# Kernel tuning notes

Hardware: AMD Instinct MI355X
Metric: run time of the kernel (lower is better)

Reference implementation:

```python
import jax, jax.numpy as jnp
import numpy as np

N_NODES = 50000
N_EDGES = 800000
N_FEAT = 256
HIDDEN = 128
N_CLASSES = 40


def gcn_conv(x, src, dst, W, b, n_nodes):
    """PyG GCNConv: add self-loops, symmetric normalization, x@W then scatter-add."""
    h = x @ W  # [N, out]
    loop = jnp.arange(n_nodes, dtype=src.dtype)
    s = jnp.concatenate([src, loop])  # [E+N]
    d = jnp.concatenate([dst, loop])
    deg = jax.ops.segment_sum(jnp.ones_like(d, dtype=h.dtype), d, num_segments=n_nodes)
    dinv = jnp.where(deg > 0, jax.lax.rsqrt(deg), 0.0)
    norm = dinv[s] * dinv[d]  # [E+N]
    msg = h[s] * norm[:, None]  # gather + scale
    out = jax.ops.segment_sum(msg, d, num_segments=n_nodes)  # scatter-add to targets
    return out + b


def setup_inputs() -> dict:
    key = jax.random.key(0)
    k1, k2, k3, k4 = jax.random.split(key, 4)
    x = jax.random.normal(k1, (N_NODES, N_FEAT), dtype=jnp.float32)
    edge_index = jax.random.randint(k2, (2, N_EDGES), 0, N_NODES, dtype=jnp.int32)
    # Glorot-style init for conv weights, zero bias (PyG default)
    W1 = jax.random.normal(k3, (N_FEAT, HIDDEN), dtype=jnp.float32) * (1.0 / np.sqrt(N_FEAT))
    b1 = jnp.zeros((HIDDEN,), dtype=jnp.float32)
    W2 = jax.random.normal(k4, (HIDDEN, N_CLASSES), dtype=jnp.float32) * (1.0 / np.sqrt(HIDDEN))
    b2 = jnp.zeros((N_CLASSES,), dtype=jnp.float32)
    return {"x": x, "edge_index": edge_index, "W1": W1, "b1": b1, "W2": W2, "b2": b2}


def reference(x, edge_index, W1, b1, W2, b2):
    # eval mode: dropout is identity
    src, dst = edge_index[0], edge_index[1]
    h = gcn_conv(x, src, dst, W1, b1, N_NODES)
    h = jax.nn.relu(h)
    h = gcn_conv(h, src, dst, W2, b2, N_NODES)
    return jax.nn.log_softmax(h, axis=1)
```

## Files before the change

kernel.cpp:

```cpp
#include <hip/hip_runtime.h>
#include <cstdint>

#define N_NODES 50000
#define N_EDGES 800000
#define N_FEAT 256
#define HIDDEN 128
#define N_CLASSES 40
#define NBUCKET 196
#define EPB 3125
#define ROWS_PAD 50048
#define H2S 64

typedef __attribute__((ext_vector_type(8))) short bf16x8;
typedef __attribute__((ext_vector_type(4))) float f32x4;

__device__ inline ushort f2bf(float f) {
    union { float f; uint u; } v; v.f = f;
    uint u = v.u;
    u += 0x7fff + ((u >> 16) & 1);
    return (ushort)(u >> 16);
}
__device__ inline float bflo(uint u) {
    union { uint u; float f; } v; v.u = u << 16; return v.f;
}
__device__ inline float bfhi(uint u) {
    union { uint u; float f; } v; v.u = u & 0xffff0000u; return v.f;
}


__global__ void hist_repack(const int* __restrict__ dst, int* __restrict__ histT,
                            const float* __restrict__ W1, const float* __restrict__ W2,
                            ushort* __restrict__ Bp1, ushort* __restrict__ Bp2) {
    __shared__ int h[NBUCKET];
    int blk = blockIdx.x, t = threadIdx.x;
    int gid = blk * 256 + t;
    if (gid < 32768) {
        int j = gid & 7, lane = (gid >> 3) & 63, kt = (gid >> 9) & 7, nt = gid >> 12;
        int k = kt * 32 + (lane >> 4) * 8 + j;
        int n = nt * 16 + (lane & 15);
        Bp1[gid] = f2bf(W1[k * HIDDEN + n]);
    } else if (gid < 32768 + 6144) {
        int i2 = gid - 32768;
        int j = i2 & 7, lane = (i2 >> 3) & 63, kt = (i2 >> 9) & 3, nt = i2 >> 11;
        int k = kt * 32 + (lane >> 4) * 8 + j;
        int n = nt * 16 + (lane & 15);
        Bp2[i2] = (n < N_CLASSES) ? f2bf(W2[k * N_CLASSES + n]) : (ushort)0;
    }
    if (t < NBUCKET) h[t] = 0;
    __syncthreads();
    int base = blk * EPB;
    for (int i = t; i < EPB; i += 256)
        atomicAdd(&h[dst[base + i] >> 8], 1);
    __syncthreads();
    if (t < NBUCKET) histT[t * 256 + blk] = h[t];
}


__global__ void scan_a(const int* __restrict__ in, int* __restrict__ incl,
                       int* __restrict__ bsum) {
    __shared__ int s[256];
    int blk = blockIdx.x, t = threadIdx.x;
    int i = blk * 256 + t;
    s[t] = in[i];
    __syncthreads();
    for (int off = 1; off < 256; off <<= 1) {
        int t2 = 0;
        if (t >= off) t2 = s[t - off];
        __syncthreads();
        s[t] += t2;
        __syncthreads();
    }
    incl[i] = s[t];
    if (t == 255) bsum[blk] = s[255];
}

__global__ void scan_c(int* __restrict__ incl, const int* __restrict__ in,
                       const int* __restrict__ bsum) {
    __shared__ int s[256];
    int blk = blockIdx.x, t = threadIdx.x;
    s[t] = (t < NBUCKET) ? bsum[t] : 0;
    __syncthreads();
    for (int off = 1; off < 256; off <<= 1) {
        int t2 = 0;
        if (t >= off) t2 = s[t - off];
        __syncthreads();
        s[t] += t2;
        __syncthreads();
    }
    int base = (blk > 0) ? s[blk - 1] : 0;
    int i = blk * 256 + t;
    incl[i] = incl[i] - in[i] + base;
}


__global__ void partition_k(const int* __restrict__ src, const int* __restrict__ dst,
                            const int* __restrict__ poff, uint* __restrict__ ebuf) {
    __shared__ int base[NBUCKET];
    __shared__ int cur[NBUCKET];
    int blk = blockIdx.x, t = threadIdx.x;
    if (t < NBUCKET) { base[t] = poff[t * 256 + blk]; cur[t] = 0; }
    __syncthreads();
    int eb = blk * EPB;
    for (int i = t; i < EPB; i += 256) {
        int d = dst[eb + i], s = src[eb + i];
        int bk = d >> 8;
        int p = base[bk] + atomicAdd(&cur[bk], 1);
        ebuf[p] = ((uint)d << 16) | (uint)s;
    }
}


__global__ void bucket_csr(const uint* __restrict__ ebuf, const int* __restrict__ poff,
                           int* __restrict__ deg, float* __restrict__ dinv,
                           int* __restrict__ rowptr, int* __restrict__ esrc) {
    __shared__ int cnt[256];
    __shared__ int s[256];
    __shared__ int exc[256];
    __shared__ int cur[256];
    int b = blockIdx.x, t = threadIdx.x;
    cnt[t] = 0;
    cur[t] = 0;
    __syncthreads();
    int beg = poff[b * 256];
    int end = (b < NBUCKET - 1) ? poff[(b + 1) * 256] : N_EDGES;
    for (int i = beg + t; i < end; i += 256)
        atomicAdd(&cnt[(ebuf[i] >> 16) & 255], 1);
    __syncthreads();
    int d = cnt[t];
    s[t] = d;
    __syncthreads();
    for (int off = 1; off < 256; off <<= 1) {
        int t2 = 0;
        if (t >= off) t2 = s[t - off];
        __syncthreads();
        s[t] += t2;
        __syncthreads();
    }
    exc[t] = s[t] - d;
    int node = b * 256 + t;
    if (node < N_NODES) {
        deg[node] = d;
        dinv[node] = rsqrtf((float)(d + 1));
        rowptr[node] = beg + exc[t];
    }
    __syncthreads();
    for (int i = beg + t; i < end; i += 256) {
        uint u = ebuf[i];
        int dl = (int)(u >> 16) & 255;
        int pos = beg + exc[dl] + atomicAdd(&cur[dl], 1);
        esrc[pos] = (int)(u & 0xffffu);
    }
}


#define XS_STRIDE 264

__global__ __launch_bounds__(256) void gemm1_mfma(const float* __restrict__ x,
                                                  const ushort* __restrict__ Bp,
                                                  ushort* __restrict__ h1b) {
    __shared__ ushort xs[64 * XS_STRIDE];
    int t = threadIdx.x;
    int row0 = blockIdx.x * 64;
#pragma unroll
    for (int i = 0; i < 16; ++i) {
        int idx = t + i * 256;
        int r = idx >> 6, kg = idx & 63;
        int row = row0 + r;
        float4 v = make_float4(0.f, 0.f, 0.f, 0.f);
        if (row < N_NODES) v = *(const float4*)(x + (size_t)row * N_FEAT + kg * 4);
        ushort4 u;
        u.x = f2bf(v.x); u.y = f2bf(v.y); u.z = f2bf(v.z); u.w = f2bf(v.w);
        *(ushort4*)(&xs[r * XS_STRIDE + kg * 4]) = u;
    }
    __syncthreads();
    int lane = t & 63, w = t >> 6;
    int r = lane & 15, q = lane >> 4;
    f32x4 acc[8] = {};
    for (int kt = 0; kt < 8; ++kt) {
        bf16x8 a = *(const bf16x8*)(&xs[(w * 16 + r) * XS_STRIDE + kt * 32 + q * 8]);
#pragma unroll
        for (int nt = 0; nt < 8; ++nt) {
            bf16x8 b = *(const bf16x8*)(Bp + (((nt * 8 + kt) * 64) + lane) * 8);
            acc[nt] = __builtin_amdgcn_mfma_f32_16x16x32_bf16(a, b, acc[nt], 0, 0, 0);
        }
    }
#pragma unroll
    for (int nt = 0; nt < 8; ++nt) {
        int col = nt * 16 + r;
#pragma unroll
        for (int reg = 0; reg < 4; ++reg) {
            int row = row0 + w * 16 + q * 4 + reg;
            if (row < N_NODES) h1b[(size_t)row * HIDDEN + col] = f2bf(acc[nt][reg]);
        }
    }
}


__global__ void agg1_g(const int* __restrict__ rowptr, const int* __restrict__ deg,
                       const int* __restrict__ esrc, const float* __restrict__ dinv,
                       const ushort* __restrict__ h1b, const float* __restrict__ b1,
                       ushort* __restrict__ hagb) {
    int w = threadIdx.x >> 6, lane = threadIdx.x & 63;
    int v = blockIdx.x * 4 + w;
    if (v >= N_NODES) return;
    int half = lane >> 5, l = lane & 31;
    int beg = rowptr[v], d = deg[v];
    float dv = dinv[v];
    float ax = 0.f, ay = 0.f, az = 0.f, aw = 0.f;
    if (half == 0) {
        uint2 hv = *(const uint2*)(h1b + (size_t)v * HIDDEN + l * 4);
        float dd = dv * dv;
        ax = bflo(hv.x) * dd; ay = bfhi(hv.x) * dd;
        az = bflo(hv.y) * dd; aw = bfhi(hv.y) * dd;
    }
    int e_l = (lane < d) ? esrc[beg + lane] : 0;
    float w_l = (lane < d) ? dinv[e_l] : 0.f;
    int dm = min(d, 64);
    int i = 0;
    for (; i + 4 <= dm; i += 4) {
        int s0 = __shfl(e_l, i + half, 64);
        int s1 = __shfl(e_l, i + 2 + half, 64);
        float g0 = __shfl(w_l, i + half, 64) * dv;
        float g1 = __shfl(w_l, i + 2 + half, 64) * dv;
        uint2 h0 = *(const uint2*)(h1b + (size_t)s0 * HIDDEN + l * 4);
        uint2 h1v = *(const uint2*)(h1b + (size_t)s1 * HIDDEN + l * 4);
        ax = fmaf(bflo(h0.x), g0, ax);  ay = fmaf(bfhi(h0.x), g0, ay);
        az = fmaf(bflo(h0.y), g0, az);  aw = fmaf(bfhi(h0.y), g0, aw);
        ax = fmaf(bflo(h1v.x), g1, ax); ay = fmaf(bfhi(h1v.x), g1, ay);
        az = fmaf(bflo(h1v.y), g1, az); aw = fmaf(bfhi(h1v.y), g1, aw);
    }
    for (; i < dm; i += 2) {
        int s0 = __shfl(e_l, i + half, 64);
        float g0 = __shfl(w_l, i + half, 64) * dv;
        uint2 h0 = *(const uint2*)(h1b + (size_t)s0 * HIDDEN + l * 4);
        ax = fmaf(bflo(h0.x), g0, ax); ay = fmaf(bfhi(h0.x), g0, ay);
        az = fmaf(bflo(h0.y), g0, az); aw = fmaf(bfhi(h0.y), g0, aw);
    }
    for (int j = 64 + half; j < d; j += 2) {
        int s = esrc[beg + j];
        float g = dinv[s] * dv;
        uint2 hs = *(const uint2*)(h1b + (size_t)s * HIDDEN + l * 4);
        ax = fmaf(bflo(hs.x), g, ax); ay = fmaf(bfhi(hs.x), g, ay);
        az = fmaf(bflo(hs.y), g, az); aw = fmaf(bfhi(hs.y), g, aw);
    }
    ax += __shfl_xor(ax, 32, 64);
    ay += __shfl_xor(ay, 32, 64);
    az += __shfl_xor(az, 32, 64);
    aw += __shfl_xor(aw, 32, 64);
    if (half == 0) {
        float4 bb = ((const float4*)b1)[l];
        ax += bb.x; ay += bb.y; az += bb.z; aw += bb.w;
        ax = ax > 0.f ? ax : 0.f;
        ay = ay > 0.f ? ay : 0.f;
        az = az > 0.f ? az : 0.f;
        aw = aw > 0.f ? aw : 0.f;
        uint2 o;
        o.x = ((uint)f2bf(ay) << 16) | (uint)f2bf(ax);
        o.y = ((uint)f2bf(aw) << 16) | (uint)f2bf(az);
        *(uint2*)(hagb + (size_t)v * HIDDEN + l * 4) = o;
    }
}


__global__ __launch_bounds__(256) void gemm2_mfma(const ushort* __restrict__ hagb,
                                                  const ushort* __restrict__ Bp,
                                                  ushort* __restrict__ h2b) {
    int t = threadIdx.x;
    int lane = t & 63, w = t >> 6;
    int r = lane & 15, q = lane >> 4;
    int row0 = blockIdx.x * 64;
    int arow = row0 + w * 16 + r;
    f32x4 acc[3] = {};
    for (int kt = 0; kt < 4; ++kt) {
        bf16x8 a = *(const bf16x8*)(hagb + (size_t)arow * HIDDEN + kt * 32 + q * 8);
#pragma unroll
        for (int nt = 0; nt < 3; ++nt) {
            bf16x8 b = *(const bf16x8*)(Bp + (((nt * 4 + kt) * 64) + lane) * 8);
            acc[nt] = __builtin_amdgcn_mfma_f32_16x16x32_bf16(a, b, acc[nt], 0, 0, 0);
        }
    }
#pragma unroll
    for (int nt = 0; nt < 3; ++nt) {
        int col = nt * 16 + r;
        if (col >= N_CLASSES) continue;
#pragma unroll
        for (int reg = 0; reg < 4; ++reg) {
            int row = row0 + w * 16 + q * 4 + reg;
            if (row < N_NODES) h2b[(size_t)row * H2S + col] = f2bf(acc[nt][reg]);
        }
    }
}


__global__ void agg2_lsm(const int* __restrict__ rowptr, const int* __restrict__ deg,
                         const int* __restrict__ esrc, const float* __restrict__ dinv,
                         const ushort* __restrict__ h2b, const float* __restrict__ b2,
                         float* __restrict__ out) {
    int t = threadIdx.x;
    int w = t >> 6, lane = t & 63;
    int half = lane >> 5, l = lane & 31;
    int v = blockIdx.x * 8 + w * 2 + half;
    int beg = rowptr[v], d = deg[v];
    float dv = dinv[v];
    float ax = 0.f, ay = 0.f;
    if (l < 20) {
        uint hv = *(const uint*)(h2b + (size_t)v * H2S + l * 2);
        ax = bflo(hv) * dv * dv;
        ay = bfhi(hv) * dv * dv;
    }
    int e_l = (l < d) ? esrc[beg + l] : 0;
    float w_l = (l < d) ? dinv[e_l] : 0.f;
    int dm = min(d, 32);
    int base = half * 32;
    int i = 0;
    for (; i + 4 <= dm; i += 4) {
        int s0 = __shfl(e_l, base + i + 0, 64);
        int s1 = __shfl(e_l, base + i + 1, 64);
        int s2 = __shfl(e_l, base + i + 2, 64);
        int s3 = __shfl(e_l, base + i + 3, 64);
        float g0 = __shfl(w_l, base + i + 0, 64) * dv;
        float g1 = __shfl(w_l, base + i + 1, 64) * dv;
        float g2 = __shfl(w_l, base + i + 2, 64) * dv;
        float g3 = __shfl(w_l, base + i + 3, 64) * dv;
        if (l < 20) {
            uint h0 = *(const uint*)(h2b + (size_t)s0 * H2S + l * 2);
            uint h1 = *(const uint*)(h2b + (size_t)s1 * H2S + l * 2);
            uint h2 = *(const uint*)(h2b + (size_t)s2 * H2S + l * 2);
            uint h3 = *(const uint*)(h2b + (size_t)s3 * H2S + l * 2);
            ax = fmaf(bflo(h0), g0, ax); ay = fmaf(bfhi(h0), g0, ay);
            ax = fmaf(bflo(h1), g1, ax); ay = fmaf(bfhi(h1), g1, ay);
            ax = fmaf(bflo(h2), g2, ax); ay = fmaf(bfhi(h2), g2, ay);
            ax = fmaf(bflo(h3), g3, ax); ay = fmaf(bfhi(h3), g3, ay);
        }
    }
    for (; i < dm; ++i) {
        int s = __shfl(e_l, base + i, 64);
        float g = __shfl(w_l, base + i, 64) * dv;
        if (l < 20) {
            uint hs = *(const uint*)(h2b + (size_t)s * H2S + l * 2);
            ax = fmaf(bflo(hs), g, ax);
            ay = fmaf(bfhi(hs), g, ay);
        }
    }
    for (i = 32; i < d; ++i) {
        int s = esrc[beg + i];
        float g = dinv[s] * dv;
        if (l < 20) {
            uint hs = *(const uint*)(h2b + (size_t)s * H2S + l * 2);
            ax = fmaf(bflo(hs), g, ax);
            ay = fmaf(bfhi(hs), g, ay);
        }
    }
    if (l < 20) {
        float2 bb = ((const float2*)b2)[l];
        ax += bb.x; ay += bb.y;
    }
    float m = (l < 20) ? fmaxf(ax, ay) : -INFINITY;
#pragma unroll
    for (int off = 16; off; off >>= 1) m = fmaxf(m, __shfl_xor(m, off, 64));
    float e = (l < 20) ? (expf(ax - m) + expf(ay - m)) : 0.f;
#pragma unroll
    for (int off = 16; off; off >>= 1) e += __shfl_xor(e, off, 64);
    float ls = logf(e);
    if (l < 20) {
        float2 o;
        o.x = ax - m - ls;
        o.y = ay - m - ls;
        ((float2*)(out + (size_t)v * N_CLASSES))[l] = o;
    }
}


extern "C" void kernel_launch(void* const* d_in, const int* in_sizes, int n_in,
                              void* d_out, int out_size, void* d_ws, size_t ws_size,
                              hipStream_t stream) {
    const float* x  = (const float*)d_in[0];
    const int*   ei = (const int*)d_in[1];
    const float* W1 = (const float*)d_in[2];
    const float* b1 = (const float*)d_in[3];
    const float* W2 = (const float*)d_in[4];
    const float* b2 = (const float*)d_in[5];
    const int* src = ei;
    const int* dst = ei + N_EDGES;
    float* out = (float*)d_out;

    char* ws = (char*)d_ws;
    size_t off = 0;
    auto alloc = [&](size_t bytes) {
        void* p = ws + off;
        off += (bytes + 255) & ~(size_t)255;
        return p;
    };
    int*    deg    = (int*)alloc((size_t)N_NODES * 4);
    float*  dinv   = (float*)alloc((size_t)N_NODES * 4);
    int*    histT  = (int*)alloc((size_t)NBUCKET * 256 * 4);
    int*    poff   = (int*)alloc((size_t)NBUCKET * 256 * 4);
    int*    rowptr = (int*)alloc((size_t)N_NODES * 4);
    int*    bsumA  = (int*)alloc((size_t)256 * 4);
    uint*   ebuf   = (uint*)alloc((size_t)N_EDGES * 4);
    int*    esrc   = (int*)alloc((size_t)N_EDGES * 4);
    ushort* Bp1    = (ushort*)alloc((size_t)32768 * 2);
    ushort* Bp2    = (ushort*)alloc((size_t)6144 * 2);
    ushort* h1b    = (ushort*)alloc((size_t)ROWS_PAD * HIDDEN * 2);
    ushort* hagb   = (ushort*)alloc((size_t)ROWS_PAD * HIDDEN * 2);
    ushort* h2b    = (ushort*)alloc((size_t)ROWS_PAD * H2S * 2);

    hist_repack<<<256, 256, 0, stream>>>(dst, histT, W1, W2, Bp1, Bp2);
    scan_a<<<NBUCKET, 256, 0, stream>>>(histT, poff, bsumA);
    scan_c<<<NBUCKET, 256, 0, stream>>>(poff, histT, bsumA);
    partition_k<<<256, 256, 0, stream>>>(src, dst, poff, ebuf);
    bucket_csr<<<NBUCKET, 256, 0, stream>>>(ebuf, poff, deg, dinv, rowptr, esrc);

    gemm1_mfma<<<ROWS_PAD / 64, 256, 0, stream>>>(x, Bp1, h1b);
    agg1_g<<<(N_NODES + 3) / 4, 256, 0, stream>>>(rowptr, deg, esrc, dinv, h1b, b1, hagb);
    gemm2_mfma<<<ROWS_PAD / 64, 256, 0, stream>>>(hagb, Bp2, h2b);
    agg2_lsm<<<N_NODES / 8, 256, 0, stream>>>(rowptr, deg, esrc, dinv, h2b, b2, out);
}
```

Measured before the change: 202.3 us.

## Fuse scan_c into partition/bucket kernels and fuse gemm2 into agg1

Removes the scan_c kernel by recomputing the bucket-sum prefix scan inside partition_k and bucket_csr, which now derive per-block offsets as inclusive minus histogram plus bucket start. It also fuses the second GEMM into the first aggregation kernel. Each block loads W2 (20 KB fp32) into shared memory and computes the 40 output classes per node with scalar FMAs, so the hagb intermediate and its round trip through memory are gone, along with two kernel launches. In exchange, every agg1 block reloads W2 and uses 20+ KB of LDS, which can reduce occupancy. The second GEMM also now runs in fp32 scalar code instead of bf16 MFMA.

```diff
diff --git a/kernel.cpp b/kernel.cpp
--- a/kernel.cpp
+++ b/kernel.cpp
@@ -29,8 +29,7 @@
 
 
 __global__ void hist_repack(const int* __restrict__ dst, int* __restrict__ histT,
-                            const float* __restrict__ W1, const float* __restrict__ W2,
-                            ushort* __restrict__ Bp1, ushort* __restrict__ Bp2) {
+                            const float* __restrict__ W1, ushort* __restrict__ Bp1) {
     __shared__ int h[NBUCKET];
     int blk = blockIdx.x, t = threadIdx.x;
     int gid = blk * 256 + t;
@@ -39,12 +38,6 @@
         int k = kt * 32 + (lane >> 4) * 8 + j;
         int n = nt * 16 + (lane & 15);
         Bp1[gid] = f2bf(W1[k * HIDDEN + n]);
-    } else if (gid < 32768 + 6144) {
-        int i2 = gid - 32768;
-        int j = i2 & 7, lane = (i2 >> 3) & 63, kt = (i2 >> 9) & 3, nt = i2 >> 11;
-        int k = kt * 32 + (lane >> 4) * 8 + j;
-        int n = nt * 16 + (lane & 15);
-        Bp2[i2] = (n < N_CLASSES) ? f2bf(W2[k * N_CLASSES + n]) : (ushort)0;
     }
     if (t < NBUCKET) h[t] = 0;
     __syncthreads();
@@ -74,8 +67,12 @@
     if (t == 255) bsum[blk] = s[255];
 }
 
-__global__ void scan_c(int* __restrict__ incl, const int* __restrict__ in,
-                       const int* __restrict__ bsum) {
+
+__global__ void partition_k(const int* __restrict__ src, const int* __restrict__ dst,
+                            const int* __restrict__ incl, const int* __restrict__ hist,
+                            const int* __restrict__ bsum, uint* __restrict__ ebuf) {
+    __shared__ int ebase[NBUCKET];
+    __shared__ int cur[NBUCKET];
     __shared__ int s[256];
     int blk = blockIdx.x, t = threadIdx.x;
     s[t] = (t < NBUCKET) ? bsum[t] : 0;
@@ -87,30 +84,23 @@
         s[t] += t2;
         __syncthreads();
     }
-    int base = (blk > 0) ? s[blk - 1] : 0;
-    int i = blk * 256 + t;
-    incl[i] = incl[i] - in[i] + base;
-}
-
-
-__global__ void partition_k(const int* __restrict__ src, const int* __restrict__ dst,
-                            const int* __restrict__ poff, uint* __restrict__ ebuf) {
-    __shared__ int base[NBUCKET];
-    __shared__ int cur[NBUCKET];
-    int blk = blockIdx.x, t = threadIdx.x;
-    if (t < NBUCKET) { base[t] = poff[t * 256 + blk]; cur[t] = 0; }
+    if (t < NBUCKET) {
+        int bucket_start = (t > 0) ? s[t - 1] : 0;
+        ebase[t] = bucket_start + incl[t * 256 + blk] - hist[t * 256 + blk];
+        cur[t] = 0;
+    }
     __syncthreads();
     int eb = blk * EPB;
     for (int i = t; i < EPB; i += 256) {
-        int d = dst[eb + i], s = src[eb + i];
+        int d = dst[eb + i], sv = src[eb + i];
         int bk = d >> 8;
-        int p = base[bk] + atomicAdd(&cur[bk], 1);
-        ebuf[p] = ((uint)d << 16) | (uint)s;
-    }
-}
-
-
-__global__ void bucket_csr(const uint* __restrict__ ebuf, const int* __restrict__ poff,
+        int p = ebase[bk] + atomicAdd(&cur[bk], 1);
+        ebuf[p] = ((uint)d << 16) | (uint)sv;
+    }
+}
+
+
+__global__ void bucket_csr(const uint* __restrict__ ebuf, const int* __restrict__ bsum,
                            int* __restrict__ deg, float* __restrict__ dinv,
                            int* __restrict__ rowptr, int* __restrict__ esrc) {
     __shared__ int cnt[256];
@@ -118,11 +108,21 @@
     __shared__ int exc[256];
     __shared__ int cur[256];
     int b = blockIdx.x, t = threadIdx.x;
+    s[t] = (t < NBUCKET) ? bsum[t] : 0;
+    __syncthreads();
+    for (int off = 1; off < 256; off <<= 1) {
+        int t2 = 0;
+        if (t >= off) t2 = s[t - off];
+        __syncthreads();
+        s[t] += t2;
+        __syncthreads();
+    }
+    int beg = (b > 0) ? s[b - 1] : 0;
+    int end = s[b];
+    __syncthreads();
     cnt[t] = 0;
     cur[t] = 0;
     __syncthreads();
-    int beg = poff[b * 256];
-    int end = (b < NBUCKET - 1) ? poff[(b + 1) * 256] : N_EDGES;
     for (int i = beg + t; i < end; i += 256)
         atomicAdd(&cnt[(ebuf[i] >> 16) & 255], 1);
     __syncthreads();
@@ -196,13 +196,19 @@
 }
 
 
-__global__ void agg1_g(const int* __restrict__ rowptr, const int* __restrict__ deg,
-                       const int* __restrict__ esrc, const float* __restrict__ dinv,
-                       const ushort* __restrict__ h1b, const float* __restrict__ b1,
-                       ushort* __restrict__ hagb) {
-    int w = threadIdx.x >> 6, lane = threadIdx.x & 63;
+__global__ __launch_bounds__(256) void agg1_gemm2(
+        const int* __restrict__ rowptr, const int* __restrict__ deg,
+        const int* __restrict__ esrc, const float* __restrict__ dinv,
+        const ushort* __restrict__ h1b, const float* __restrict__ b1,
+        const float* __restrict__ W2, ushort* __restrict__ h2b) {
+    __shared__ float Ws[HIDDEN * N_CLASSES];
+    __shared__ float rowbuf[4][HIDDEN];
+    int t = threadIdx.x;
+    for (int i = t; i < HIDDEN * N_CLASSES / 4; i += 256)
+        ((float4*)Ws)[i] = ((const float4*)W2)[i];
+
+    int w = t >> 6, lane = t & 63;
     int v = blockIdx.x * 4 + w;
-    if (v >= N_NODES) return;
     int half = lane >> 5, l = lane & 31;
     int beg = rowptr[v], d = deg[v];
     float dv = dinv[v];
@@ -250,44 +256,20 @@
     if (half == 0) {
         float4 bb = ((const float4*)b1)[l];
         ax += bb.x; ay += bb.y; az += bb.z; aw += bb.w;
-        ax = ax > 0.f ? ax : 0.f;
-        ay = ay > 0.f ? ay : 0.f;
-        az = az > 0.f ? az : 0.f;
-        aw = aw > 0.f ? aw : 0.f;
-        uint2 o;
-        o.x = ((uint)f2bf(ay) << 16) | (uint)f2bf(ax);
-        o.y = ((uint)f2bf(aw) << 16) | (uint)f2bf(az);
-        *(uint2*)(hagb + (size_t)v * HIDDEN + l * 4) = o;
-    }
-}
-
-
-__global__ __launch_bounds__(256) void gemm2_mfma(const ushort* __restrict__ hagb,
-                                                  const ushort* __restrict__ Bp,
-                                                  ushort* __restrict__ h2b) {
-    int t = threadIdx.x;
-    int lane = t & 63, w = t >> 6;
-    int r = lane & 15, q = lane >> 4;
-    int row0 = blockIdx.x * 64;
-    int arow = row0 + w * 16 + r;
-    f32x4 acc[3] = {};
-    for (int kt = 0; kt < 4; ++kt) {
-        bf16x8 a = *(const bf16x8*)(hagb + (size_t)arow * HIDDEN + kt * 32 + q * 8);
-#pragma unroll
-        for (int nt = 0; nt < 3; ++nt) {
-            bf16x8 b = *(const bf16x8*)(Bp + (((nt * 4 + kt) * 64) + lane) * 8);
-            acc[nt] = __builtin_amdgcn_mfma_f32_16x16x32_bf16(a, b, acc[nt], 0, 0, 0);
-        }
-    }
-#pragma unroll
-    for (int nt = 0; nt < 3; ++nt) {
-        int col = nt * 16 + r;
-        if (col >= N_CLASSES) continue;
-#pragma unroll
-        for (int reg = 0; reg < 4; ++reg) {
-            int row = row0 + w * 16 + q * 4 + reg;
-            if (row < N_NODES) h2b[(size_t)row * H2S + col] = f2bf(acc[nt][reg]);
-        }
+        float4 r;
+        r.x = ax > 0.f ? ax : 0.f;
+        r.y = ay > 0.f ? ay : 0.f;
+        r.z = az > 0.f ? az : 0.f;
+        r.w = aw > 0.f ? aw : 0.f;
+        *(float4*)(&rowbuf[w][l * 4]) = r;
+    }
+    __syncthreads();
+    if (lane < N_CLASSES) {
+        float acc = 0.f;
+#pragma unroll 8
+        for (int k = 0; k < HIDDEN; ++k)
+            acc = fmaf(rowbuf[w][k], Ws[k * N_CLASSES + lane], acc);
+        h2b[(size_t)v * H2S + lane] = f2bf(acc);
     }
 }
 
@@ -394,25 +376,21 @@
     int*    deg    = (int*)alloc((size_t)N_NODES * 4);
     float*  dinv   = (float*)alloc((size_t)N_NODES * 4);
     int*    histT  = (int*)alloc((size_t)NBUCKET * 256 * 4);
-    int*    poff   = (int*)alloc((size_t)NBUCKET * 256 * 4);
+    int*    incl   = (int*)alloc((size_t)NBUCKET * 256 * 4);
     int*    rowptr = (int*)alloc((size_t)N_NODES * 4);
-    int*    bsumA  = (int*)alloc((size_t)256 * 4);
+    int*    bsum   = (int*)alloc((size_t)256 * 4);
     uint*   ebuf   = (uint*)alloc((size_t)N_EDGES * 4);
     int*    esrc   = (int*)alloc((size_t)N_EDGES * 4);
     ushort* Bp1    = (ushort*)alloc((size_t)32768 * 2);
-    ushort* Bp2    = (ushort*)alloc((size_t)6144 * 2);
     ushort* h1b    = (ushort*)alloc((size_t)ROWS_PAD * HIDDEN * 2);
-    ushort* hagb   = (ushort*)alloc((size_t)ROWS_PAD * HIDDEN * 2);
     ushort* h2b    = (ushort*)alloc((size_t)ROWS_PAD * H2S * 2);
 
-    hist_repack<<<256, 256, 0, stream>>>(dst, histT, W1, W2, Bp1, Bp2);
-    scan_a<<<NBUCKET, 256, 0, stream>>>(histT, poff, bsumA);
-    scan_c<<<NBUCKET, 256, 0, stream>>>(poff, histT, bsumA);
-    partition_k<<<256, 256, 0, stream>>>(src, dst, poff, ebuf);
-    bucket_csr<<<NBUCKET, 256, 0, stream>>>(ebuf, poff, deg, dinv, rowptr, esrc);
+    hist_repack<<<256, 256, 0, stream>>>(dst, histT, W1, Bp1);
+    scan_a<<<NBUCKET, 256, 0, stream>>>(histT, incl, bsum);
+    partition_k<<<256, 256, 0, stream>>>(src, dst, incl, histT, bsum, ebuf);
+    bucket_csr<<<NBUCKET, 256, 0, stream>>>(ebuf, bsum, deg, dinv, rowptr, esrc);
 
     gemm1_mfma<<<ROWS_PAD / 64, 256, 0, stream>>>(x, Bp1, h1b);
-    agg1_g<<<(N_NODES + 3) / 4, 256, 0, stream>>>(rowptr, deg, esrc, dinv, h1b, b1, hagb);
-    gemm2_mfma<<<ROWS_PAD / 64, 256, 0, stream>>>(hagb, Bp2, h2b);
+    agg1_gemm2<<<N_NODES / 4, 256, 0, stream>>>(rowptr, deg, esrc, dinv, h1b, b1, W2, h2b);
     agg2_lsm<<<N_NODES / 8, 256, 0, stream>>>(rowptr, deg, esrc, dinv, h2b, b2, out);
 }
```

After: 228.7 us. +13.0%, slower.
